# Performance work log

Measured on AMD Instinct MI355X. Metric: run time of the kernel, lower is better.

Reference implementation:

```python
import jax, jax.numpy as jnp
import numpy as np

B, S, E = 2, 2048, 1024
H = 16
D = E // H  # head dim

def setup_inputs() -> dict:
    key = jax.random.key(0)
    ks = jax.random.split(key, 9)
    s = 1.0 / np.sqrt(E)
    return {
        "hidden_states": jax.random.normal(ks[0], (B, S, E), dtype=jnp.float32),
        "Wq": jax.random.normal(ks[1], (E, E), dtype=jnp.float32) * s,
        "bq": jnp.zeros((E,), jnp.float32),
        "Wk": jax.random.normal(ks[2], (E, E), dtype=jnp.float32) * s,
        "bk": jnp.zeros((E,), jnp.float32),
        "Wv": jax.random.normal(ks[3], (E, E), dtype=jnp.float32) * s,
        "bv": jnp.zeros((E,), jnp.float32),
        "Wo": jax.random.normal(ks[4], (E, E), dtype=jnp.float32) * s,
        "bo": jnp.zeros((E,), jnp.float32),
    }

def _split_heads(x):
    # [B,S,E] -> [B,H,S,D]
    b, s, _ = x.shape
    return x.reshape(b, s, H, D).transpose(0, 2, 1, 3)

def reference(hidden_states, Wq, bq, Wk, bk, Wv, bv, Wo, bo):
    q = _split_heads(hidden_states @ Wq + bq)  # [B,H,S,D]
    k = _split_heads(hidden_states @ Wk + bk)
    v = _split_heads(hidden_states @ Wv + bv)
    scores = jnp.einsum('bhqd,bhkd->bhqk', q, k) / jnp.sqrt(jnp.float32(D))
    probs = jax.nn.softmax(scores, axis=-1)  # [B,H,S,S]
    ctx = jnp.einsum('bhqk,bhkd->bhqd', probs, v)
    ctx = ctx.transpose(0, 2, 1, 3).reshape(hidden_states.shape[0], -1, E)
    out = ctx @ Wo + bo
    return out, probs
```

## Files before the change

### kernel.cpp

```cpp
#include <hip/hip_runtime.h>
#include <hip/hip_bf16.h>
#include <stdint.h>


typedef __attribute__((ext_vector_type(8))) short bf16x8;
typedef __attribute__((ext_vector_type(4))) short bf16x4v;
typedef __attribute__((ext_vector_type(4))) float f32x4;

#define DEV static __device__ __forceinline__

DEV short f2bs(float f) {
  union { __hip_bfloat16 b; short s; } u;
  u.b = __float2bfloat16(f);
  return u.s;
}
DEV f32x4 mfma16(bf16x8 a, bf16x8 b, f32x4 c) {
  return __builtin_amdgcn_mfma_f32_16x16x32_bf16(a, b, c, 0, 0, 0);
}
DEV float fexp2(float x) { return __builtin_amdgcn_exp2f(x); }
typedef const __attribute__((address_space(1))) void* gas1_t;
typedef __attribute__((address_space(3))) void* las3_t;
DEV void gload_lds16(const void* g, void* l) {
  __builtin_amdgcn_global_load_lds((gas1_t)(uintptr_t)g, (las3_t)(uint32_t)(uintptr_t)l,
                                   16, 0, 0);
}
#define WAIT_VMCNT(N) asm volatile("s_waitcnt vmcnt(" #N ")" ::: "memory")
#define WAIT_LGKM0() asm volatile("s_waitcnt lgkmcnt(0)" ::: "memory")
#define BARRIER() do { __builtin_amdgcn_s_barrier(); __builtin_amdgcn_sched_barrier(0); } while (0)

__global__ void cvt_all_kernel(const float* __restrict__ X,
                               const float* __restrict__ Wq, const float* __restrict__ Wk,
                               const float* __restrict__ Wv, const float* __restrict__ Wo,
                               short* __restrict__ Xb, short* __restrict__ Wt) {
  __shared__ short tile[64][68];
  int bx = blockIdx.x, t = threadIdx.x;
  if (bx < 2048) {
    size_t i = (size_t)bx * 256 + t;
    const float4* X4 = (const float4*)X;
    float4 a = X4[2 * i], c = X4[2 * i + 1];
    bf16x8 o;
    o[0] = f2bs(a.x); o[1] = f2bs(a.y); o[2] = f2bs(a.z); o[3] = f2bs(a.w);
    o[4] = f2bs(c.x); o[5] = f2bs(c.y); o[6] = f2bs(c.z); o[7] = f2bs(c.w);
    *(bf16x8*)(Xb + i * 8) = o;
    return;
  }
  int wb = bx - 2048;
  int mat = wb >> 8, rem = wb & 255;
  const float* W = mat == 0 ? Wq : mat == 1 ? Wk : mat == 2 ? Wv : Wo;
  int kb = (rem >> 4) * 64, nb = (rem & 15) * 64;
#pragma unroll
  for (int it = 0; it < 4; ++it) {
    int idx = it * 256 + t;
    int row = idx >> 4, c4 = (idx & 15) * 4;
    float4 v = *(const float4*)(W + (size_t)(kb + row) * 1024 + nb + c4);
    tile[row][c4 + 0] = f2bs(v.x); tile[row][c4 + 1] = f2bs(v.y);
    tile[row][c4 + 2] = f2bs(v.z); tile[row][c4 + 3] = f2bs(v.w);
  }
  __syncthreads();
#pragma unroll
  for (int it = 0; it < 4; ++it) {
    int idx = it * 256 + t;
    int rn = idx >> 4, c4 = (idx & 15) * 4;
    bf16x4v o;
    o[0] = tile[c4 + 0][rn]; o[1] = tile[c4 + 1][rn];
    o[2] = tile[c4 + 2][rn]; o[3] = tile[c4 + 3][rn];
    *(bf16x4v*)(Wt + (((size_t)mat) << 20) + (size_t)(nb + rn) * 1024 + kb + c4) = o;
  }
}

template <int MODE, int GBX>
__global__ __launch_bounds__(256, MODE == 0 ? 2 : 3)
void gemm_bt_kernel(const short* __restrict__ A, const short* __restrict__ Bt,
                    const float* __restrict__ bias0, const float* __restrict__ bias1,
                    const float* __restrict__ bias2,
                    short* __restrict__ o0, short* __restrict__ o1, short* __restrict__ o2,
                    float* __restrict__ fout) {
  constexpr int BN = (MODE == 0) ? 128 : 64;
  constexpr int NBLINES = BN / 32;
  __shared__ short As[2][128 * 64];
  __shared__ short Bs[2][BN * 64];
  const int nwg = GBX * gridDim.y;
  const int cpx = nwg >> 3;
  const int bid0 = blockIdx.y * GBX + blockIdx.x;
  const int bid = (bid0 % 8) * cpx + bid0 / 8;
  const int m0 = (bid % GBX) * 128, n0 = (bid / GBX) * BN;
  const int t = threadIdx.x, w = t >> 6, l = t & 63, g = l >> 4, r = l & 15;
  const int lr = l >> 3, lc = l & 7;
  const int swz = lc ^ lr;
  const int wr = (w >> 1) * 64, wc = (w & 1) * (BN / 2);
  f32x4 acc[4][BN / 32] = {};

#define STAGE_G(k0_, b_)                                                                \
  do {                                                                                  \
    _Pragma("unroll") for (int it_ = 0; it_ < 4; ++it_)                                 \
        gload_lds16(A + (size_t)(m0 + it_ * 32 + w * 8 + lr) * 1024 + (k0_) + swz * 8,  \
                    As[b_] + (it_ * 32 + w * 8) * 64);                                  \
    _Pragma("unroll") for (int it_ = 0; it_ < NBLINES; ++it_)                           \
        gload_lds16(Bt + (size_t)(n0 + it_ * 32 + w * 8 + lr) * 1024 + (k0_) + swz * 8, \
                    Bs[b_] + (it_ * 32 + w * 8) * 64);                                  \
  } while (0)

  STAGE_G(0, 0);
  for (int it = 0; it < 16; ++it) {
    const int cur = it & 1;
    if (it < 15) {
      STAGE_G((it + 1) * 64, cur ^ 1);
      if constexpr (MODE == 0) { WAIT_VMCNT(8); } else { WAIT_VMCNT(6); }
    } else {
      WAIT_VMCNT(0);
    }
    BARRIER();
    bf16x8 af[2][4], bfv[2][BN / 32];
#pragma unroll
    for (int df = 0; df < 2; df++) {
#pragma unroll
      for (int i = 0; i < 4; i++)
        af[df][i] = *(const bf16x8*)(As[cur] + (wr + i * 16 + r) * 64 +
                                     ((df * 4 + g) ^ (r & 7)) * 8);
#pragma unroll
      for (int j = 0; j < BN / 32; j++)
        bfv[df][j] = *(const bf16x8*)(Bs[cur] + (wc + j * 16 + r) * 64 +
                                      ((df * 4 + g) ^ (r & 7)) * 8);
    }
    __builtin_amdgcn_s_setprio(1);
#pragma unroll
    for (int df = 0; df < 2; df++)
#pragma unroll
      for (int i = 0; i < 4; i++)
#pragma unroll
        for (int j = 0; j < BN / 32; j++)
          acc[i][j] = mfma16(af[df][i], bfv[df][j], acc[i][j]);
    __builtin_amdgcn_s_setprio(0);
    BARRIER();
  }
#undef STAGE_G
  if constexpr (MODE == 0) {
#pragma unroll
    for (int j = 0; j < 4; j++) {
      int ng = n0 + wc + j * 16 + r;
      int mat = ng >> 10, nn = ng & 1023, hh = nn >> 6, dd = nn & 63;
      const float* bp = mat == 0 ? bias0 : (mat == 1 ? bias1 : bias2);
      short* dst = mat == 0 ? o0 : (mat == 1 ? o1 : o2);
      float bv = bp[nn];
      float sc = (mat == 0) ? 0.18033688f : 1.0f;
#pragma unroll
      for (int i = 0; i < 4; i++) {
#pragma unroll
        for (int q = 0; q < 4; q++) {
          int m = m0 + wr + i * 16 + g * 4 + q;
          int bb = m >> 11, ss = m & 2047;
          dst[((size_t)(bb * 16 + hh) * 2048 + ss) * 64 + dd] = f2bs((acc[i][j][q] + bv) * sc);
        }
      }
    }
  } else {
#pragma unroll
    for (int i = 0; i < 4; i++)
#pragma unroll
      for (int q = 0; q < 4; q++) {
        int m = m0 + wr + i * 16 + g * 4 + q;
#pragma unroll
        for (int j = 0; j < 2; j++) {
          int ng = n0 + wc + j * 16 + r;
          fout[(size_t)m * 1024 + ng] = acc[i][j][q] + bias0[ng];
        }
      }
  }
}

__global__ __launch_bounds__(256, 2)
void attn_kernel(const short* __restrict__ Qm, const short* __restrict__ Km,
                 const short* __restrict__ Vm, float* __restrict__ probs,
                 short* __restrict__ ctx) {
  __shared__ short Ks[2][128 * 64];
  __shared__ short Vt[64 * 136];
  __shared__ short Ps[4][16 * 136];
  __shared__ float rls[128];
  const int f = blockIdx.x;
  const int wgid = (f & 7) * 64 + (f >> 3);
  const int bh = wgid >> 4, q0 = (wgid & 15) * 128;
  const int bb = bh >> 4, hh = bh & 15;
  const short* Qp = Qm + (size_t)bh * 2048 * 64;
  const short* Kp = Km + (size_t)bh * 2048 * 64;
  const short* Vp = Vm + (size_t)bh * 2048 * 64;
  float* Pp = probs + (size_t)bh * 2048 * 2048;
  const int t = threadIdx.x, w = t >> 6, l = t & 63, g = l >> 4, r = l & 15;
  const int lr = l >> 3, lc = l & 7;
  const int swz = lc ^ lr;

#define STAGE_K(kt_, buf_)                                                            \
  do {                                                                                \
    const short* src_ = Kp + (size_t)((kt_) * 128) * 64;                              \
    _Pragma("unroll") for (int it_ = 0; it_ < 4; ++it_)                               \
        gload_lds16(src_ + (size_t)(it_ * 32 + w * 8 + lr) * 64 + swz * 8,            \
                    Ks[buf_] + (it_ * 32 + w * 8) * 64);                              \
  } while (0)

#pragma unroll
  for (int it = 0; it < 2; ++it) {
    gload_lds16(Qp + (size_t)(q0 + it * 32 + w * 8 + lr) * 64 + swz * 8,
                Ks[0] + (it * 32 + w * 8) * 64);
    gload_lds16(Qp + (size_t)(q0 + 64 + it * 32 + w * 8 + lr) * 64 + swz * 8,
                Ks[1] + (it * 32 + w * 8) * 64);
  }
  __syncthreads();
  bf16x8 qf0[2], qf1[2];
#pragma unroll
  for (int df = 0; df < 2; df++) {
    qf0[df] = *(const bf16x8*)(Ks[0] + (w * 16 + r) * 64 + ((df * 4 + g) ^ (r & 7)) * 8);
    qf1[df] = *(const bf16x8*)(Ks[1] + (w * 16 + r) * 64 + ((df * 4 + g) ^ (r & 7)) * 8);
  }
  WAIT_LGKM0();
  BARRIER();

  float lrow0 = 0.f;
  STAGE_K(0, 0);
  for (int kt = 0; kt < 16; ++kt) {
    const int cur = kt & 1;
    if (kt < 15) {
      STAGE_K(kt + 1, cur ^ 1);
      WAIT_VMCNT(4);
    } else {
      WAIT_VMCNT(0);
    }
    BARRIER();
    f32x4 st[8] = {};
    __builtin_amdgcn_s_setprio(1);
#pragma unroll
    for (int df = 0; df < 2; ++df) {
      bf16x8 kf[8];
#pragma unroll
      for (int ni = 0; ni < 8; ni++)
        kf[ni] = *(const bf16x8*)(Ks[cur] + (ni * 16 + r) * 64 + ((df * 4 + g) ^ (r & 7)) * 8);
#pragma unroll
      for (int ni = 0; ni < 8; ni++) st[ni] = mfma16(kf[ni], qf0[df], st[ni]);
    }
    __builtin_amdgcn_s_setprio(0);
    float ssum = 0.f;
#pragma unroll
    for (int ni = 0; ni < 8; ni++)
#pragma unroll
      for (int q4 = 0; q4 < 4; q4++) ssum += fexp2(st[ni][q4]);
    ssum += __shfl_xor(ssum, 16);
    ssum += __shfl_xor(ssum, 32);
    lrow0 += ssum;
    BARRIER();
  }
  const float rinv0 = 1.0f / lrow0;
  if (g == 0) rls[w * 16 + r] = rinv0;

  const int kp = (t >> 3) * 2, d0v = (t & 7) * 8, lcv = t & 7, kunit = t >> 5;

#define B_TILE_BODY(stv_, qrow_, rinv_)                                                \
  do {                                                                                 \
                              \
    _Pragma("unroll") for (int ni = 0; ni < 8; ni++) {                                 \
      bf16x4v pk;                                                                      \
      _Pragma("unroll") for (int q4 = 0; q4 < 4; q4++) {                               \
        float pe = fexp2((stv_)[ni][q4]);                                              \
        (stv_)[ni][q4] = pe;                                                           \
        pk[q4] = f2bs(pe);                                                             \
      }                                                                                \
      *(bf16x4v*)(&Ps[w][r * 136 + ni * 16 + g * 4]) = pk;                             \
    }                                                                                  \
                               \
    _Pragma("unroll") for (int e = 0; e < 8; e++) {                                    \
      unsigned int p0_ = (unsigned int)(unsigned short)v0[e] |                         \
                         ((unsigned int)(unsigned short)v1[e] << 16);                  \
      unsigned int p1_ = (unsigned int)(unsigned short)v2[e] |                         \
                         ((unsigned int)(unsigned short)v3[e] << 16);                  \
      *(unsigned int*)(Vt + (d0v + e) * 136 + ((kunit ^ lcv) << 3) + (kp & 7)) = p0_;  \
      *(unsigned int*)(Vt + (d0v + e) * 136 + ((8 + (kunit ^ lcv)) << 3) + (kp & 7)) = p1_; \
    }                                                                                  \
    WAIT_LGKM0();                                                                      \
    BARRIER();                                                                         \
              \
    _Pragma("unroll") for (int ni = 0; ni < 8; ni++) {                                 \
      f32x4 pr;                                                                        \
      _Pragma("unroll") for (int q4 = 0; q4 < 4; q4++) pr[q4] = (stv_)[ni][q4] * (rinv_); \
      *(f32x4*)(Pp + (size_t)((qrow_) + w * 16 + r) * 2048 + kt * 128 + ni * 16 + g * 4) = pr; \
    }                                                                                  \
                             \
    __builtin_amdgcn_s_setprio(1);                                                     \
    _Pragma("unroll") for (int kf4 = 0; kf4 < 4; ++kf4) {                              \
      bf16x8 pa, vb[4];                                                                \
      pa = *(const bf16x8*)(&Ps[w][r * 136 + kf4 * 32 + g * 8]);                       \
      _Pragma("unroll") for (int nj = 0; nj < 4; nj++) {                               \
        int u_ = kf4 * 4 + g, x_ = nj * 2 + (r >> 3);                                  \
        int su_ = (u_ & 8) | ((u_ & 7) ^ x_);                                          \
        vb[nj] = *(const bf16x8*)(Vt + (nj * 16 + r) * 136 + (su_ << 3));              \
      }                                                                                \
      _Pragma("unroll") for (int nj = 0; nj < 4; nj++)                                 \
          cacc[nj] = mfma16(pa, vb[nj], cacc[nj]);                                     \
    }                                                                                  \
    __builtin_amdgcn_s_setprio(0);                                                     \
  } while (0)

  f32x4 cacc[4] = {};
  float lrow1 = 0.f;
  STAGE_K(0, 0);
  for (int kt = 0; kt < 16; ++kt) {
    const int cur = kt & 1;
    bf16x8 v0 = *(const bf16x8*)(Vp + (size_t)(kt * 128 + kp) * 64 + d0v);
    bf16x8 v1 = *(const bf16x8*)(Vp + (size_t)(kt * 128 + kp + 1) * 64 + d0v);
    bf16x8 v2 = *(const bf16x8*)(Vp + (size_t)(kt * 128 + 64 + kp) * 64 + d0v);
    bf16x8 v3 = *(const bf16x8*)(Vp + (size_t)(kt * 128 + 64 + kp + 1) * 64 + d0v);
    if (kt < 15) STAGE_K(kt + 1, cur ^ 1);
    if (kt == 0) { WAIT_VMCNT(8); }
    else if (kt < 15) { WAIT_VMCNT(16); }
    else { WAIT_VMCNT(12); }
    BARRIER();
    f32x4 st0[8] = {}, st1[8] = {};
    __builtin_amdgcn_s_setprio(1);
#pragma unroll
    for (int df = 0; df < 2; ++df) {
      bf16x8 kf[8];
#pragma unroll
      for (int ni = 0; ni < 8; ni++)
        kf[ni] = *(const bf16x8*)(Ks[cur] + (ni * 16 + r) * 64 + ((df * 4 + g) ^ (r & 7)) * 8);
#pragma unroll
      for (int ni = 0; ni < 8; ni++) {
        st0[ni] = mfma16(kf[ni], qf0[df], st0[ni]);
        st1[ni] = mfma16(kf[ni], qf1[df], st1[ni]);
      }
    }
    __builtin_amdgcn_s_setprio(0);
    {
      float ssum = 0.f;
#pragma unroll
      for (int ni = 0; ni < 8; ni++)
#pragma unroll
        for (int q4 = 0; q4 < 4; q4++) ssum += fexp2(st1[ni][q4]);
      ssum += __shfl_xor(ssum, 16);
      ssum += __shfl_xor(ssum, 32);
      lrow1 += ssum;
    }
    B_TILE_BODY(st0, q0, rinv0);
  }
#pragma unroll
  for (int nj = 0; nj < 4; nj++)
#pragma unroll
    for (int q4 = 0; q4 < 4; q4++) {
      int qt = w * 16 + g * 4 + q4;
      float val = cacc[nj][q4] * rls[qt];
      ctx[((size_t)(bb * 2048 + q0 + qt)) * 1024 + hh * 64 + nj * 16 + r] = f2bs(val);
    }

  const float rinv1 = 1.0f / lrow1;
  if (g == 0) rls[64 + w * 16 + r] = rinv1;
#pragma unroll
  for (int nj = 0; nj < 4; nj++) cacc[nj] = (f32x4){0.f, 0.f, 0.f, 0.f};
  STAGE_K(0, 0);
  for (int kt = 0; kt < 16; ++kt) {
    const int cur = kt & 1;
    bf16x8 v0 = *(const bf16x8*)(Vp + (size_t)(kt * 128 + kp) * 64 + d0v);
    bf16x8 v1 = *(const bf16x8*)(Vp + (size_t)(kt * 128 + kp + 1) * 64 + d0v);
    bf16x8 v2 = *(const bf16x8*)(Vp + (size_t)(kt * 128 + 64 + kp) * 64 + d0v);
    bf16x8 v3 = *(const bf16x8*)(Vp + (size_t)(kt * 128 + 64 + kp + 1) * 64 + d0v);
    if (kt < 15) STAGE_K(kt + 1, cur ^ 1);
    if (kt == 0) { WAIT_VMCNT(8); }
    else if (kt < 15) { WAIT_VMCNT(16); }
    else { WAIT_VMCNT(12); }
    BARRIER();
    f32x4 st[8] = {};
    __builtin_amdgcn_s_setprio(1);
#pragma unroll
    for (int df = 0; df < 2; ++df) {
      bf16x8 kf[8];
#pragma unroll
      for (int ni = 0; ni < 8; ni++)
        kf[ni] = *(const bf16x8*)(Ks[cur] + (ni * 16 + r) * 64 + ((df * 4 + g) ^ (r & 7)) * 8);
#pragma unroll
      for (int ni = 0; ni < 8; ni++) st[ni] = mfma16(kf[ni], qf1[df], st[ni]);
    }
    __builtin_amdgcn_s_setprio(0);
    B_TILE_BODY(st, q0 + 64, rinv1);
  }
#pragma unroll
  for (int nj = 0; nj < 4; nj++)
#pragma unroll
    for (int q4 = 0; q4 < 4; q4++) {
      int qt = w * 16 + g * 4 + q4;
      float val = cacc[nj][q4] * rls[64 + qt];
      ctx[((size_t)(bb * 2048 + q0 + 64 + qt)) * 1024 + hh * 64 + nj * 16 + r] = f2bs(val);
    }
#undef B_TILE_BODY
#undef STAGE_K
}

extern "C" void kernel_launch(void* const* d_in, const int* in_sizes, int n_in,
                              void* d_out, int out_size, void* d_ws, size_t ws_size,
                              hipStream_t stream) {
  (void)in_sizes; (void)n_in; (void)out_size; (void)ws_size;
  const float* X  = (const float*)d_in[0];
  const float* Wq = (const float*)d_in[1];
  const float* bq = (const float*)d_in[2];
  const float* Wk = (const float*)d_in[3];
  const float* bk = (const float*)d_in[4];
  const float* Wv = (const float*)d_in[5];
  const float* bv = (const float*)d_in[6];
  const float* Wo = (const float*)d_in[7];
  const float* bo = (const float*)d_in[8];
  float* out = (float*)d_out;
  float* probs = out + (size_t)2 * 2048 * 1024;

  short* Xb = (short*)d_ws;
  short* Wt = Xb + (size_t)4194304;
  short* Qb = Wt + (size_t)4194304;
  short* Kb = Qb + (size_t)4194304;
  short* Vb = Kb + (size_t)4194304;
  short* Cx = Vb + (size_t)4194304;

  cvt_all_kernel<<<3072, 256, 0, stream>>>(X, Wq, Wk, Wv, Wo, Xb, Wt);
  gemm_bt_kernel<0, 32><<<dim3(32, 24), 256, 0, stream>>>(Xb, Wt, bq, bk, bv,
                                                          Qb, Kb, Vb, nullptr);
  attn_kernel<<<512, 256, 0, stream>>>(Qb, Kb, Vb, probs, Cx);
  gemm_bt_kernel<1, 32><<<dim3(32, 16), 256, 0, stream>>>(Cx, Wt + (size_t)3 * 1048576, bo,
                                                          nullptr, nullptr, nullptr, nullptr,
                                                          nullptr, out);
}
```

Before: 212.8 us.

## Process both 64-row query halves together in each pass over K and V

The first pass now computes row sums for both query halves at once, and the second and third passes merge into a single loop. That loop computes scores for both halves, writes both probability tiles and accumulates both context tiles. This removes one full sweep of K and V loads plus the QK^T recompute for the second half. In exchange it raises register pressure (two score arrays, two accumulators, packed bf16 copies) and adjusts the vmcnt waits to match the extra outstanding probability stores. The two P·V products reuse one Ps buffer in sequence, with no barrier between the second Ps write and its reads, which relies on per-warp ownership of Ps[w].

```diff
diff --git a/kernel.cpp b/kernel.cpp
--- a/kernel.cpp
+++ b/kernel.cpp
@@ -213,7 +213,7 @@
   WAIT_LGKM0();
   BARRIER();
 
-  float lrow0 = 0.f;
+  float lrow0 = 0.f, lrow1 = 0.f;
   STAGE_K(0, 0);
   for (int kt = 0; kt < 16; ++kt) {
     const int cur = kt & 1;
@@ -224,7 +224,7 @@
       WAIT_VMCNT(0);
     }
     BARRIER();
-    f32x4 st[8] = {};
+    f32x4 st0[8] = {}, st1[8] = {};
     __builtin_amdgcn_s_setprio(1);
 #pragma unroll
     for (int df = 0; df < 2; ++df) {
@@ -233,71 +233,36 @@
       for (int ni = 0; ni < 8; ni++)
         kf[ni] = *(const bf16x8*)(Ks[cur] + (ni * 16 + r) * 64 + ((df * 4 + g) ^ (r & 7)) * 8);
 #pragma unroll
-      for (int ni = 0; ni < 8; ni++) st[ni] = mfma16(kf[ni], qf0[df], st[ni]);
+      for (int ni = 0; ni < 8; ni++) {
+        st0[ni] = mfma16(kf[ni], qf0[df], st0[ni]);
+        st1[ni] = mfma16(kf[ni], qf1[df], st1[ni]);
+      }
     }
     __builtin_amdgcn_s_setprio(0);
-    float ssum = 0.f;
+    float s0 = 0.f, s1 = 0.f;
 #pragma unroll
     for (int ni = 0; ni < 8; ni++)
 #pragma unroll
-      for (int q4 = 0; q4 < 4; q4++) ssum += fexp2(st[ni][q4]);
-    ssum += __shfl_xor(ssum, 16);
-    ssum += __shfl_xor(ssum, 32);
-    lrow0 += ssum;
+      for (int q4 = 0; q4 < 4; q4++) {
+        s0 += fexp2(st0[ni][q4]);
+        s1 += fexp2(st1[ni][q4]);
+      }
+    s0 += __shfl_xor(s0, 16); s0 += __shfl_xor(s0, 32);
+    s1 += __shfl_xor(s1, 16); s1 += __shfl_xor(s1, 32);
+    lrow0 += s0;
+    lrow1 += s1;
     BARRIER();
   }
   const float rinv0 = 1.0f / lrow0;
-  if (g == 0) rls[w * 16 + r] = rinv0;
+  const float rinv1 = 1.0f / lrow1;
+  if (g == 0) {
+    rls[w * 16 + r] = rinv0;
+    rls[64 + w * 16 + r] = rinv1;
+  }
 
   const int kp = (t >> 3) * 2, d0v = (t & 7) * 8, lcv = t & 7, kunit = t >> 5;
 
-#define B_TILE_BODY(stv_, qrow_, rinv_)                                                \
-  do {                                                                                 \
-                              \
-    _Pragma("unroll") for (int ni = 0; ni < 8; ni++) {                                 \
-      bf16x4v pk;                                                                      \
-      _Pragma("unroll") for (int q4 = 0; q4 < 4; q4++) {                               \
-        float pe = fexp2((stv_)[ni][q4]);                                              \
-        (stv_)[ni][q4] = pe;                                                           \
-        pk[q4] = f2bs(pe);                                                             \
-      }                                                                                \
-      *(bf16x4v*)(&Ps[w][r * 136 + ni * 16 + g * 4]) = pk;                             \
-    }                                                                                  \
-                               \
-    _Pragma("unroll") for (int e = 0; e < 8; e++) {                                    \
-      unsigned int p0_ = (unsigned int)(unsigned short)v0[e] |                         \
-                         ((unsigned int)(unsigned short)v1[e] << 16);                  \
-      unsigned int p1_ = (unsigned int)(unsigned short)v2[e] |                         \
-                         ((unsigned int)(unsigned short)v3[e] << 16);                  \
-      *(unsigned int*)(Vt + (d0v + e) * 136 + ((kunit ^ lcv) << 3) + (kp & 7)) = p0_;  \
-      *(unsigned int*)(Vt + (d0v + e) * 136 + ((8 + (kunit ^ lcv)) << 3) + (kp & 7)) = p1_; \
-    }                                                                                  \
-    WAIT_LGKM0();                                                                      \
-    BARRIER();                                                                         \
-              \
-    _Pragma("unroll") for (int ni = 0; ni < 8; ni++) {                                 \
-      f32x4 pr;                                                                        \
-      _Pragma("unroll") for (int q4 = 0; q4 < 4; q4++) pr[q4] = (stv_)[ni][q4] * (rinv_); \
-      *(f32x4*)(Pp + (size_t)((qrow_) + w * 16 + r) * 2048 + kt * 128 + ni * 16 + g * 4) = pr; \
-    }                                                                                  \
-                             \
-    __builtin_amdgcn_s_setprio(1);                                                     \
-    _Pragma("unroll") for (int kf4 = 0; kf4 < 4; ++kf4) {                              \
-      bf16x8 pa, vb[4];                                                                \
-      pa = *(const bf16x8*)(&Ps[w][r * 136 + kf4 * 32 + g * 8]);                       \
-      _Pragma("unroll") for (int nj = 0; nj < 4; nj++) {                               \
-        int u_ = kf4 * 4 + g, x_ = nj * 2 + (r >> 3);                                  \
-        int su_ = (u_ & 8) | ((u_ & 7) ^ x_);                                          \
-        vb[nj] = *(const bf16x8*)(Vt + (nj * 16 + r) * 136 + (su_ << 3));              \
-      }                                                                                \
-      _Pragma("unroll") for (int nj = 0; nj < 4; nj++)                                 \
-          cacc[nj] = mfma16(pa, vb[nj], cacc[nj]);                                     \
-    }                                                                                  \
-    __builtin_amdgcn_s_setprio(0);                                                     \
-  } while (0)
-
-  f32x4 cacc[4] = {};
-  float lrow1 = 0.f;
+  f32x4 cacc0[4] = {}, cacc1[4] = {};
   STAGE_K(0, 0);
   for (int kt = 0; kt < 16; ++kt) {
     const int cur = kt & 1;
@@ -307,8 +272,8 @@
     bf16x8 v3 = *(const bf16x8*)(Vp + (size_t)(kt * 128 + 64 + kp + 1) * 64 + d0v);
     if (kt < 15) STAGE_K(kt + 1, cur ^ 1);
     if (kt == 0) { WAIT_VMCNT(8); }
-    else if (kt < 15) { WAIT_VMCNT(16); }
-    else { WAIT_VMCNT(12); }
+    else if (kt < 15) { WAIT_VMCNT(24); }
+    else { WAIT_VMCNT(20); }
     BARRIER();
     f32x4 st0[8] = {}, st1[8] = {};
     __builtin_amdgcn_s_setprio(1);
@@ -325,66 +290,91 @@
       }
     }
     __builtin_amdgcn_s_setprio(0);
-    {
-      float ssum = 0.f;
-#pragma unroll
-      for (int ni = 0; ni < 8; ni++)
-#pragma unroll
-        for (int q4 = 0; q4 < 4; q4++) ssum += fexp2(st1[ni][q4]);
-      ssum += __shfl_xor(ssum, 16);
-      ssum += __shfl_xor(ssum, 32);
-      lrow1 += ssum;
-    }
-    B_TILE_BODY(st0, q0, rinv0);
+    bf16x4v pk0[8], pk1[8];
+#pragma unroll
+    for (int ni = 0; ni < 8; ni++) {
+#pragma unroll
+      for (int q4 = 0; q4 < 4; q4++) {
+        float p0 = fexp2(st0[ni][q4]);
+        float p1 = fexp2(st1[ni][q4]);
+        st0[ni][q4] = p0;
+        st1[ni][q4] = p1;
+        pk0[ni][q4] = f2bs(p0);
+        pk1[ni][q4] = f2bs(p1);
+      }
+    }
+#pragma unroll
+    for (int e = 0; e < 8; e++) {
+      unsigned int p0_ = (unsigned int)(unsigned short)v0[e] |
+                         ((unsigned int)(unsigned short)v1[e] << 16);
+      unsigned int p1_ = (unsigned int)(unsigned short)v2[e] |
+                         ((unsigned int)(unsigned short)v3[e] << 16);
+      *(unsigned int*)(Vt + (d0v + e) * 136 + ((kunit ^ lcv) << 3) + (kp & 7)) = p0_;
+      *(unsigned int*)(Vt + (d0v + e) * 136 + ((8 + (kunit ^ lcv)) << 3) + (kp & 7)) = p1_;
+    }
+#pragma unroll
+    for (int ni = 0; ni < 8; ni++)
+      *(bf16x4v*)(&Ps[w][r * 136 + ni * 16 + g * 4]) = pk0[ni];
+    WAIT_LGKM0();
+    BARRIER();
+#pragma unroll
+    for (int ni = 0; ni < 8; ni++) {
+      f32x4 pr;
+#pragma unroll
+      for (int q4 = 0; q4 < 4; q4++) pr[q4] = st0[ni][q4] * rinv0;
+      *(f32x4*)(Pp + (size_t)(q0 + w * 16 + r) * 2048 + kt * 128 + ni * 16 + g * 4) = pr;
+    }
+    __builtin_amdgcn_s_setprio(1);
+#pragma unroll
+    for (int kf4 = 0; kf4 < 4; ++kf4) {
+      bf16x8 pa, vb[4];
+      pa = *(const bf16x8*)(&Ps[w][r * 136 + kf4 * 32 + g * 8]);
+#pragma unroll
+      for (int nj = 0; nj < 4; nj++) {
+        int u_ = kf4 * 4 + g, x_ = nj * 2 + (r >> 3);
+        int su_ = (u_ & 8) | ((u_ & 7) ^ x_);
+        vb[nj] = *(const bf16x8*)(Vt + (nj * 16 + r) * 136 + (su_ << 3));
+      }
+#pragma unroll
+      for (int nj = 0; nj < 4; nj++) cacc0[nj] = mfma16(pa, vb[nj], cacc0[nj]);
+    }
+    __builtin_amdgcn_s_setprio(0);
+#pragma unroll
+    for (int ni = 0; ni < 8; ni++)
+      *(bf16x4v*)(&Ps[w][r * 136 + ni * 16 + g * 4]) = pk1[ni];
+#pragma unroll
+    for (int ni = 0; ni < 8; ni++) {
+      f32x4 pr;
+#pragma unroll
+      for (int q4 = 0; q4 < 4; q4++) pr[q4] = st1[ni][q4] * rinv1;
+      *(f32x4*)(Pp + (size_t)(q0 + 64 + w * 16 + r) * 2048 + kt * 128 + ni * 16 + g * 4) = pr;
+    }
+    __builtin_amdgcn_s_setprio(1);
+#pragma unroll
+    for (int kf4 = 0; kf4 < 4; ++kf4) {
+      bf16x8 pa, vb[4];
+      pa = *(const bf16x8*)(&Ps[w][r * 136 + kf4 * 32 + g * 8]);
+#pragma unroll
+      for (int nj = 0; nj < 4; nj++) {
+        int u_ = kf4 * 4 + g, x_ = nj * 2 + (r >> 3);
+        int su_ = (u_ & 8) | ((u_ & 7) ^ x_);
+        vb[nj] = *(const bf16x8*)(Vt + (nj * 16 + r) * 136 + (su_ << 3));
+      }
+#pragma unroll
+      for (int nj = 0; nj < 4; nj++) cacc1[nj] = mfma16(pa, vb[nj], cacc1[nj]);
+    }
+    __builtin_amdgcn_s_setprio(0);
   }
 #pragma unroll
   for (int nj = 0; nj < 4; nj++)
 #pragma unroll
     for (int q4 = 0; q4 < 4; q4++) {
       int qt = w * 16 + g * 4 + q4;
-      float val = cacc[nj][q4] * rls[qt];
-      ctx[((size_t)(bb * 2048 + q0 + qt)) * 1024 + hh * 64 + nj * 16 + r] = f2bs(val);
-    }
-
-  const float rinv1 = 1.0f / lrow1;
-  if (g == 0) rls[64 + w * 16 + r] = rinv1;
-#pragma unroll
-  for (int nj = 0; nj < 4; nj++) cacc[nj] = (f32x4){0.f, 0.f, 0.f, 0.f};
-  STAGE_K(0, 0);
-  for (int kt = 0; kt < 16; ++kt) {
-    const int cur = kt & 1;
-    bf16x8 v0 = *(const bf16x8*)(Vp + (size_t)(kt * 128 + kp) * 64 + d0v);
-    bf16x8 v1 = *(const bf16x8*)(Vp + (size_t)(kt * 128 + kp + 1) * 64 + d0v);
-    bf16x8 v2 = *(const bf16x8*)(Vp + (size_t)(kt * 128 + 64 + kp) * 64 + d0v);
-    bf16x8 v3 = *(const bf16x8*)(Vp + (size_t)(kt * 128 + 64 + kp + 1) * 64 + d0v);
-    if (kt < 15) STAGE_K(kt + 1, cur ^ 1);
-    if (kt == 0) { WAIT_VMCNT(8); }
-    else if (kt < 15) { WAIT_VMCNT(16); }
-    else { WAIT_VMCNT(12); }
-    BARRIER();
-    f32x4 st[8] = {};
-    __builtin_amdgcn_s_setprio(1);
-#pragma unroll
-    for (int df = 0; df < 2; ++df) {
-      bf16x8 kf[8];
-#pragma unroll
-      for (int ni = 0; ni < 8; ni++)
-        kf[ni] = *(const bf16x8*)(Ks[cur] + (ni * 16 + r) * 64 + ((df * 4 + g) ^ (r & 7)) * 8);
-#pragma unroll
-      for (int ni = 0; ni < 8; ni++) st[ni] = mfma16(kf[ni], qf1[df], st[ni]);
-    }
-    __builtin_amdgcn_s_setprio(0);
-    B_TILE_BODY(st, q0 + 64, rinv1);
-  }
-#pragma unroll
-  for (int nj = 0; nj < 4; nj++)
-#pragma unroll
-    for (int q4 = 0; q4 < 4; q4++) {
-      int qt = w * 16 + g * 4 + q4;
-      float val = cacc[nj][q4] * rls[64 + qt];
-      ctx[((size_t)(bb * 2048 + q0 + 64 + qt)) * 1024 + hh * 64 + nj * 16 + r] = f2bs(val);
-    }
-#undef B_TILE_BODY
+      float val0 = cacc0[nj][q4] * rls[qt];
+      ctx[((size_t)(bb * 2048 + q0 + qt)) * 1024 + hh * 64 + nj * 16 + r] = f2bs(val0);
+      float val1 = cacc1[nj][q4] * rls[64 + qt];
+      ctx[((size_t)(bb * 2048 + q0 + 64 + qt)) * 1024 + hh * 64 + nj * 16 + r] = f2bs(val1);
+    }
 #undef STAGE_K
 }
 
```

New measurement: 222.2 us. 1.04x slower.
